# Kernel tuning notes

Measured on AMD Instinct MI355X. Metric: run time of the kernel, lower is better.

The kernel has to match this reference:

```python
import jax, jax.numpy as jnp
from jax import lax
import numpy as np

NEG_INF = -1000000000.0  # matches torch masked_fill value
POS_THRESH = -100000000.0


def setup_inputs() -> dict:
    key = jax.random.key(0)
    k1, k2, k3 = jax.random.split(key, 3)
    B, C_in, L = 1, 16, 2048
    C_out, groups, K = 16, 4, 3
    scores = jax.random.normal(k1, (B, C_in, L, L), dtype=jnp.float32)
    weight = jax.random.normal(k2, (C_out, C_in // groups, K, K), dtype=jnp.float32) * 0.1
    bias = jax.random.normal(k3, (C_out,), dtype=jnp.float32) * 0.1
    return {"scores": scores, "weight": weight, "bias": bias}


def reference(scores, weight, bias):
    B, C_in, L, _ = scores.shape
    C_out, cpg, K, _ = weight.shape
    groups = C_in // cpg
    mask = jnp.tril(jnp.ones((L, L), dtype=bool))[None, None]  # (1,1,L,L) causal

    s = scores.astype(jnp.float32)
    z = jnp.where(mask, s, NEG_INF)

    # sparsemax over last axis: sort desc, cumsum, support-size threshold
    z_sorted = -jnp.sort(-z, axis=-1)                 # descending
    cum_sum = jnp.cumsum(z_sorted, axis=-1)
    k_idx = jnp.arange(1, L + 1, dtype=z.dtype)        # (L,) broadcasts over (B,C,L,L)
    cond = (1.0 + k_idx * z_sorted > cum_sum) & (z_sorted > POS_THRESH)
    k_sp = jnp.sum(cond, axis=-1, keepdims=True)       # support size, int
    k_safe = jnp.maximum(k_sp, 1)
    cum_sum_k = jnp.take_along_axis(cum_sum, k_safe - 1, axis=-1)
    tau = (cum_sum_k - 1.0) / k_safe.astype(z.dtype)
    tau = jnp.where(k_sp == 0, jnp.inf, tau)
    probs = jnp.maximum(z - tau, 0.0)                  # (B,C_in,L,L)

    # grouped same-padded conv2d over the (L,L) score map
    out = lax.conv_general_dilated(
        probs, weight,
        window_strides=(1, 1),
        padding=[(K // 2, K // 2), (K // 2, K // 2)],
        feature_group_count=groups,
        dimension_numbers=("NCHW", "OIHW", "NCHW"),
    )
    out = out + bias[None, :, None, None]
    out = jnp.where(mask, out, 0.0)
    return out.astype(scores.dtype)
```

## Files before the change

kernel.cpp:

```cpp
#include <hip/hip_runtime.h>

#define L 2048
#define CIN 16
#define GROUPS 4
#define NEG_INF  -1000000000.0f
#define POS_THRESH -100000000.0f

__global__ __launch_bounds__(256) void tau_kernel(const float* __restrict__ scores,
                                                  float* __restrict__ tau_out) {
    const int wid  = (blockIdx.x << 2) + (threadIdx.x >> 6);
    const int lane = threadIdx.x & 63;
    const int ws   = threadIdx.x >> 6;
    const int ch   = wid >> 11;
    const int row  = wid & 2047;
    const int n    = row + 1;
    const float* zrow = scores + ((size_t)ch * L + row) * L;

    float v[32];
    float m = NEG_INF;
#pragma unroll
    for (int j = 0; j < 8; ++j) {
        int c4 = lane + (j << 6);
        int c  = c4 << 2;
        float4 z = make_float4(NEG_INF, NEG_INF, NEG_INF, NEG_INF);
        if (c < n) z = *((const float4*)zrow + c4);
        v[4*j+0] = (c + 0 < n) ? z.x : NEG_INF;
        v[4*j+1] = (c + 1 < n) ? z.y : NEG_INF;
        v[4*j+2] = (c + 2 < n) ? z.z : NEG_INF;
        v[4*j+3] = (c + 3 < n) ? z.w : NEG_INF;
        m = fmaxf(m, fmaxf(fmaxf(v[4*j+0], v[4*j+1]), fmaxf(v[4*j+2], v[4*j+3])));
    }
#pragma unroll
    for (int d = 32; d; d >>= 1) m = fmaxf(m, __shfl_xor(m, d, 64));

    const float thr = m - 1.0f;

    __shared__ float buf[4][64];
    int base = 0;
#pragma unroll
    for (int j = 0; j < 32; ++j) {
        bool p = v[j] > thr;
        unsigned long long mask = __ballot(p);
        if (mask) {
            if (p) {
                int pos = __builtin_amdgcn_mbcnt_lo((unsigned)mask, 0);
                pos = __builtin_amdgcn_mbcnt_hi((unsigned)(mask >> 32), pos);
                pos += base;
                if (pos < 64) buf[ws][pos] = v[j];
            }
            base += __popcll(mask);
        }
    }
    __syncthreads();
    const int cnt = base;

    float tau;
    if (cnt <= 64) {
        float x = (lane < cnt) ? buf[ws][lane] : NEG_INF;
#pragma unroll
        for (int k = 2; k <= 64; k <<= 1) {
#pragma unroll
            for (int j = k >> 1; j > 0; j >>= 1) {
                float p = __shfl_xor(x, j, 64);
                bool desc    = ((lane & k) == 0);
                bool earlier = ((lane & j) == 0);
                float mx = fmaxf(x, p), mn = fminf(x, p);
                x = (desc == earlier) ? mx : mn;
            }
        }
        float csum = x;
#pragma unroll
        for (int d = 1; d < 64; d <<= 1) {
            float y = __shfl_up(csum, d, 64);
            if (lane >= d) csum += y;
        }
        bool cond = (1.0f + (float)(lane + 1) * x > csum) && (x > POS_THRESH);
        unsigned long long cmask = __ballot(cond);
        int k = (int)__popcll(cmask);
        float ck = __shfl(csum, k - 1, 64);
        tau = (ck - 1.0f) / (float)k;
    } else {
        tau = thr;
        int k_prev = -1;
        for (int it = 0; it < 64; ++it) {
            float S = 0.0f, Kf = 0.0f;
#pragma unroll
            for (int j = 0; j < 32; ++j)
                if (v[j] > tau) { S += v[j]; Kf += 1.0f; }
#pragma unroll
            for (int d = 32; d; d >>= 1) {
                S  += __shfl_xor(S,  d, 64);
                Kf += __shfl_xor(Kf, d, 64);
            }
            int K = (int)Kf;
            if (K == k_prev) break;
            tau = (S - 1.0f) / Kf;
            k_prev = K;
        }
    }
    if (lane == 0) tau_out[ch * L + row] = tau;
}

#define TR 16
#define TC 64
#define HR 18
#define PST 68

struct W6 { float l, m0, m1, m2, m3, r; };

__global__ __launch_bounds__(256, 8) void conv_kernel(const float* __restrict__ scores,
                                                      const float* __restrict__ tau,
                                                      const float* __restrict__ weight,
                                                      const float* __restrict__ bias,
                                                      float* __restrict__ out) {
    const int c0 = blockIdx.x * TC;
    const int r0 = blockIdx.y * TR;
    const int g  = blockIdx.z;
    const int t  = threadIdx.x;

    if (c0 > r0 + TR - 1) {
        const float4 z4 = make_float4(0.f, 0.f, 0.f, 0.f);
#pragma unroll
        for (int jj = 0; jj < 4; ++jj) {
            int idx = t + (jj << 8);
            int c4  = idx & 15;
            int r   = (idx >> 4) & 15;
            int o   = idx >> 8;
            float4* p = (float4*)(out + (((size_t)((g << 2) + o) * L + (r0 + r)) * L + c0)) + c4;
            *p = z4;
        }
        return;
    }

    __shared__ __align__(16) float P[4][HR][PST];

    const bool interior = (c0 >= 1) && (c0 + TC + 1 <= r0) && (r0 + TR <= L - 1);

    const float* sbase = scores + (size_t)(g << 2) * L * L;
    const float* tbase = tau + (g << 2) * L;

    float4 zr[5];
    float  tvr[5];

    if (interior) {
#pragma unroll
        for (int jj = 0; jj < 5; ++jj) {
            int idx = t + (jj << 8);
            if (idx < 1152) {
                int hr = idx >> 6, ic = (idx >> 4) & 3, c4 = idx & 15;
                int r  = r0 - 1 + hr;
                zr[jj]  = *((const float4*)(sbase + (size_t)ic * L * L + (size_t)r * L + c0) + c4);
                tvr[jj] = tbase[ic * L + r];
            }
        }
        float hv = 0.f;
        int hic = 0, hhr = 0, hside = 0;
        if (t < 144) {
            hside = t & 1;
            int j = t >> 1;
            hic = j / HR; hhr = j - hic * HR;
            int r = r0 - 1 + hhr;
            int c = hside ? (c0 + TC) : (c0 - 1);
            hv = fmaxf(sbase[(size_t)hic * L * L + (size_t)r * L + c] - tbase[hic * L + r], 0.f);
        }
#pragma unroll
        for (int jj = 0; jj < 5; ++jj) {
            int idx = t + (jj << 8);
            if (idx < 1152) {
                int hr = idx >> 6, ic = (idx >> 4) & 3, c4 = idx & 15;
                float tv = tvr[jj];
                float4 z = zr[jj];
                float4 val;
                val.x = fmaxf(z.x - tv, 0.f);
                val.y = fmaxf(z.y - tv, 0.f);
                val.z = fmaxf(z.z - tv, 0.f);
                val.w = fmaxf(z.w - tv, 0.f);
                *((float4*)&P[ic][hr][c4 << 2]) = val;
            }
        }
        if (t < 144) P[hic][hhr][hside ? TC : 67] = hv;
    } else {
#pragma unroll
        for (int jj = 0; jj < 5; ++jj) {
            int idx = t + (jj << 8);
            zr[jj] = make_float4(0.f, 0.f, 0.f, 0.f);
            tvr[jj] = 0.f;
            if (idx < 1152) {
                int hr = idx >> 6, ic = (idx >> 4) & 3, c4 = idx & 15;
                int r  = r0 - 1 + hr;
                int cb = c0 + (c4 << 2);
                if (r >= 0 && r < L && cb <= r) {
                    zr[jj]  = *((const float4*)(sbase + (size_t)ic * L * L + (size_t)r * L) + (cb >> 2));
                    tvr[jj] = tbase[ic * L + r];
                }
            }
        }
        float hv = 0.f;
        int hic = 0, hhr = 0, hside = 0;
        if (t < 144) {
            hside = t & 1;
            int j = t >> 1;
            hic = j / HR; hhr = j - hic * HR;
            int r = r0 - 1 + hhr;
            int c = hside ? (c0 + TC) : (c0 - 1);
            if (r >= 0 && r < L && c >= 0 && c <= r)
                hv = fmaxf(sbase[(size_t)hic * L * L + (size_t)r * L + c] - tbase[hic * L + r], 0.f);
        }
#pragma unroll
        for (int jj = 0; jj < 5; ++jj) {
            int idx = t + (jj << 8);
            if (idx < 1152) {
                int hr = idx >> 6, ic = (idx >> 4) & 3, c4 = idx & 15;
                int r  = r0 - 1 + hr;
                int cb = c0 + (c4 << 2);
                float tv = tvr[jj];
                float4 z = zr[jj];
                float4 val = make_float4(0.f, 0.f, 0.f, 0.f);
                if (r >= 0 && r < L && cb <= r) {
                    val.x = fmaxf(z.x - tv, 0.f);
                    val.y = (cb + 1 <= r) ? fmaxf(z.y - tv, 0.f) : 0.f;
                    val.z = (cb + 2 <= r) ? fmaxf(z.z - tv, 0.f) : 0.f;
                    val.w = (cb + 3 <= r) ? fmaxf(z.w - tv, 0.f) : 0.f;
                }
                *((float4*)&P[ic][hr][c4 << 2]) = val;
            }
        }
        if (t < 144) P[hic][hhr][hside ? TC : 67] = hv;
    }
    __syncthreads();

    const int o    = __builtin_amdgcn_readfirstlane(t >> 6);
    const int lane = t & 63;
    const int col4 = lane & 15;
    const int rq   = lane >> 4;
    const int hb   = rq << 2;
    const int go   = (g << 2) + o;
    const int cb   = c0 + (col4 << 2);
    const int li   = col4 ? ((col4 << 2) - 2) : 66;
    const int ri   = (col4 << 2) + 4;

    float w[4][9];
#pragma unroll
    for (int ic = 0; ic < 4; ++ic)
#pragma unroll
        for (int k = 0; k < 9; ++k) w[ic][k] = weight[((go << 2) + ic) * 9 + k];
    const float bb = bias[go];

    auto ldwin = [&](int ic, int hr) -> W6 {
        const float* rp = &P[ic][hr][0];
        float4 M  = *(const float4*)(rp + (col4 << 2));
        float2 Lv = *(const float2*)(rp + li);
        float2 Rv = *(const float2*)(rp + ri);
        W6 q; q.l = Lv.y; q.m0 = M.x; q.m1 = M.y; q.m2 = M.z; q.m3 = M.w; q.r = Rv.x;
        return q;
    };

    float4 acc[4];
#pragma unroll
    for (int rr = 0; rr < 4; ++rr) acc[rr] = make_float4(bb, bb, bb, bb);

#pragma unroll
    for (int ic = 0; ic < 4; ++ic) {
        W6 a = ldwin(ic, hb);
        W6 b = ldwin(ic, hb + 1);
#pragma unroll
        for (int rr = 0; rr < 4; ++rr) {
            W6 c = ldwin(ic, hb + rr + 2);
            const W6 rows[3] = { a, b, c };
#pragma unroll
            for (int dy = 0; dy < 3; ++dy) {
                const W6& q = rows[dy];
                const float w0 = w[ic][dy * 3 + 0];
                const float w1 = w[ic][dy * 3 + 1];
                const float w2 = w[ic][dy * 3 + 2];
                acc[rr].x = fmaf(q.l,  w0, fmaf(q.m0, w1, fmaf(q.m1, w2, acc[rr].x)));
                acc[rr].y = fmaf(q.m0, w0, fmaf(q.m1, w1, fmaf(q.m2, w2, acc[rr].y)));
                acc[rr].z = fmaf(q.m1, w0, fmaf(q.m2, w1, fmaf(q.m3, w2, acc[rr].z)));
                acc[rr].w = fmaf(q.m2, w0, fmaf(q.m3, w1, fmaf(q.r,  w2, acc[rr].w)));
            }
            a = b; b = c;
        }
    }

    float* outp = out + ((size_t)go * L + (r0 + hb)) * L + cb;
    if (interior) {
#pragma unroll
        for (int rr = 0; rr < 4; ++rr)
            *(float4*)(outp + (size_t)rr * L) = acc[rr];
    } else {
#pragma unroll
        for (int rr = 0; rr < 4; ++rr) {
            int r = r0 + hb + rr;
            float4 res;
            res.x = (cb     <= r) ? acc[rr].x : 0.f;
            res.y = (cb + 1 <= r) ? acc[rr].y : 0.f;
            res.z = (cb + 2 <= r) ? acc[rr].z : 0.f;
            res.w = (cb + 3 <= r) ? acc[rr].w : 0.f;
            *(float4*)(outp + (size_t)rr * L) = res;
        }
    }
}

extern "C" void kernel_launch(void* const* d_in, const int* in_sizes, int n_in,
                              void* d_out, int out_size, void* d_ws, size_t ws_size,
                              hipStream_t stream) {
    const float* scores = (const float*)d_in[0];
    const float* weight = (const float*)d_in[1];
    const float* bias   = (const float*)d_in[2];
    float* out = (float*)d_out;
    float* tau = (float*)d_ws;

    tau_kernel<<<(CIN * L) / 4, 256, 0, stream>>>(scores, tau);

    dim3 gridB(L / TC, L / TR, GROUPS);
    conv_kernel<<<gridB, 256, 0, stream>>>(scores, tau, weight, bias, out);
}
```

Before: 496.3 us.

## Remap conv threads so each computes all four output channels for one row

Each thread previously computed four consecutive output rows for one output channel, reusing sliding windows of LDS rows. Now each wave covers four rows and each thread computes all four output channels of its group for a single row, loading three LDS windows per input channel and reusing them across output channels. This reduces LDS reads per FMA and makes weight loads wave-uniform, so they can become scalar loads. In exchange, the weight loads move inside the input-channel loop.

```diff
diff --git a/kernel.cpp b/kernel.cpp
--- a/kernel.cpp
+++ b/kernel.cpp
@@ -229,22 +229,15 @@
     }
     __syncthreads();
 
-    const int o    = __builtin_amdgcn_readfirstlane(t >> 6);
+    const int w4   = t >> 6;
     const int lane = t & 63;
     const int col4 = lane & 15;
-    const int rq   = lane >> 4;
-    const int hb   = rq << 2;
-    const int go   = (g << 2) + o;
+    const int rloc = lane >> 4;
+    const int ro   = (w4 << 2) + rloc;
+    const int obase = g << 2;
     const int cb   = c0 + (col4 << 2);
     const int li   = col4 ? ((col4 << 2) - 2) : 66;
     const int ri   = (col4 << 2) + 4;
-
-    float w[4][9];
-#pragma unroll
-    for (int ic = 0; ic < 4; ++ic)
-#pragma unroll
-        for (int k = 0; k < 9; ++k) w[ic][k] = weight[((go << 2) + ic) * 9 + k];
-    const float bb = bias[go];
 
     auto ldwin = [&](int ic, int hr) -> W6 {
         const float* rp = &P[ic][hr][0];
@@ -257,46 +250,52 @@
 
     float4 acc[4];
 #pragma unroll
-    for (int rr = 0; rr < 4; ++rr) acc[rr] = make_float4(bb, bb, bb, bb);
+    for (int oc = 0; oc < 4; ++oc) {
+        float bb = bias[obase + oc];
+        acc[oc] = make_float4(bb, bb, bb, bb);
+    }
+
+#define ROWFMA(q, wa, wb, wc, A)                                           \
+    A.x = fmaf(q.l,  wa, fmaf(q.m0, wb, fmaf(q.m1, wc, A.x)));             \
+    A.y = fmaf(q.m0, wa, fmaf(q.m1, wb, fmaf(q.m2, wc, A.y)));             \
+    A.z = fmaf(q.m1, wa, fmaf(q.m2, wb, fmaf(q.m3, wc, A.z)));             \
+    A.w = fmaf(q.m2, wa, fmaf(q.m3, wb, fmaf(q.r,  wc, A.w)));
 
 #pragma unroll
     for (int ic = 0; ic < 4; ++ic) {
-        W6 a = ldwin(ic, hb);
-        W6 b = ldwin(ic, hb + 1);
-#pragma unroll
-        for (int rr = 0; rr < 4; ++rr) {
-            W6 c = ldwin(ic, hb + rr + 2);
-            const W6 rows[3] = { a, b, c };
-#pragma unroll
-            for (int dy = 0; dy < 3; ++dy) {
-                const W6& q = rows[dy];
-                const float w0 = w[ic][dy * 3 + 0];
-                const float w1 = w[ic][dy * 3 + 1];
-                const float w2 = w[ic][dy * 3 + 2];
-                acc[rr].x = fmaf(q.l,  w0, fmaf(q.m0, w1, fmaf(q.m1, w2, acc[rr].x)));
-                acc[rr].y = fmaf(q.m0, w0, fmaf(q.m1, w1, fmaf(q.m2, w2, acc[rr].y)));
-                acc[rr].z = fmaf(q.m1, w0, fmaf(q.m2, w1, fmaf(q.m3, w2, acc[rr].z)));
-                acc[rr].w = fmaf(q.m2, w0, fmaf(q.m3, w1, fmaf(q.r,  w2, acc[rr].w)));
-            }
-            a = b; b = c;
-        }
-    }
-
-    float* outp = out + ((size_t)go * L + (r0 + hb)) * L + cb;
+        W6 q0 = ldwin(ic, ro);
+        W6 q1 = ldwin(ic, ro + 1);
+        W6 q2 = ldwin(ic, ro + 2);
+#pragma unroll
+        for (int oc = 0; oc < 4; ++oc) {
+            const float* wp = weight + (((obase + oc) << 2) + ic) * 9;
+            const float w00 = wp[0], w01 = wp[1], w02 = wp[2];
+            const float w10 = wp[3], w11 = wp[4], w12 = wp[5];
+            const float w20 = wp[6], w21 = wp[7], w22 = wp[8];
+            ROWFMA(q0, w00, w01, w02, acc[oc])
+            ROWFMA(q1, w10, w11, w12, acc[oc])
+            ROWFMA(q2, w20, w21, w22, acc[oc])
+        }
+    }
+#undef ROWFMA
+
+    const int r_out = r0 + ro;
     if (interior) {
 #pragma unroll
-        for (int rr = 0; rr < 4; ++rr)
-            *(float4*)(outp + (size_t)rr * L) = acc[rr];
+        for (int oc = 0; oc < 4; ++oc) {
+            float* outp = out + ((size_t)(obase + oc) * L + r_out) * L + cb;
+            *(float4*)outp = acc[oc];
+        }
     } else {
 #pragma unroll
-        for (int rr = 0; rr < 4; ++rr) {
-            int r = r0 + hb + rr;
+        for (int oc = 0; oc < 4; ++oc) {
             float4 res;
-            res.x = (cb     <= r) ? acc[rr].x : 0.f;
-            res.y = (cb + 1 <= r) ? acc[rr].y : 0.f;
-            res.z = (cb + 2 <= r) ? acc[rr].z : 0.f;
-            res.w = (cb + 3 <= r) ? acc[rr].w : 0.f;
-            *(float4*)(outp + (size_t)rr * L) = res;
+            res.x = (cb     <= r_out) ? acc[oc].x : 0.f;
+            res.y = (cb + 1 <= r_out) ? acc[oc].y : 0.f;
+            res.z = (cb + 2 <= r_out) ? acc[oc].z : 0.f;
+            res.w = (cb + 3 <= r_out) ? acc[oc].w : 0.f;
+            float* outp = out + ((size_t)(obase + oc) * L + r_out) * L + cb;
+            *(float4*)outp = res;
         }
     }
 }
```

Measured after the change: 530.9 us. 1.07x slower.
